# Kernel tuning notes

Hardware: AMD Instinct MI355X
Metric: run time of the kernel (lower is better)

The kernel has to match this reference:

```python
import jax, jax.numpy as jnp
import numpy as np

NUM_HEADS = 8
NEG_INF = -1e30  # stand-in for float('-inf') in masked_fill; avoids NaN rows under autodiff
LN_EPS = 1e-5


def setup_inputs() -> dict:
    key = jax.random.key(0)
    ks = jax.random.split(key, 12)
    B, C, H, W = 1, 256, 64, 64
    N = H * W
    s = 1.0 / np.sqrt(C)
    inp = {
        'x': jax.random.normal(ks[0], (B, C, H, W), jnp.float32),
        'mask': jax.random.uniform(ks[1], (B, NUM_HEADS, N, N)) < 0.5,
        'Wq': jax.random.normal(ks[2], (C, C), jnp.float32) * s,
        'bq': jax.random.normal(ks[3], (C,), jnp.float32) * 0.02,
        'Wk': jax.random.normal(ks[4], (C, C), jnp.float32) * s,
        'bk': jax.random.normal(ks[5], (C,), jnp.float32) * 0.02,
        'Wv': jax.random.normal(ks[6], (C, C), jnp.float32) * s,
        'bv': jax.random.normal(ks[7], (C,), jnp.float32) * 0.02,
        'Wo': jax.random.normal(ks[8], (C, C), jnp.float32) * s,
        'bo': jax.random.normal(ks[9], (C,), jnp.float32) * 0.02,
        'gamma': jnp.ones((C,), jnp.float32),
        'beta': jnp.zeros((C,), jnp.float32),
    }
    return inp


def reference(x, mask, Wq, bq, Wk, bk, Wv, bv, Wo, bo, gamma, beta):
    B, C, H, W = x.shape
    hd = C // NUM_HEADS
    N = H * W
    scale = hd ** -0.5

    def proj(Wm, bm):
        # 1x1 conv == per-pixel channel matmul; reshape to (B, heads, N, head_dim)
        y = jnp.einsum('oc,bchw->bohw', Wm, x) + bm[None, :, None, None]
        return y.reshape(B, NUM_HEADS, hd, N).swapaxes(2, 3)

    q = proj(Wq, bq)
    k = proj(Wk, bk)
    v = proj(Wv, bv)

    scores = jnp.einsum('bhnd,bhmd->bhnm', q, k) * scale  # (B, heads, N, N)
    scores = jnp.where(mask, scores, NEG_INF)
    probs = jax.nn.softmax(scores, axis=-1)
    # dropout is identity in eval mode
    out = jnp.einsum('bhnm,bhmd->bhnd', probs, v)
    out = out.swapaxes(2, 3).reshape(B, C, H, W)
    out = jnp.einsum('oc,bchw->bohw', Wo, out) + bo[None, :, None, None]

    z = (x + out).transpose(0, 2, 3, 1)  # (B, H, W, C) for channel-last LayerNorm
    mu = jnp.mean(z, axis=-1, keepdims=True)
    var = jnp.var(z, axis=-1, keepdims=True)
    z = (z - mu) * jax.lax.rsqrt(var + LN_EPS) * gamma + beta
    return z.transpose(0, 3, 1, 2)
```

## Files before the change

### kernel.cpp

```cpp
#include <hip/hip_runtime.h>


#define NH 8
#define CC 256
#define NN 4096
#define HD 32
#define KSPLIT 4

typedef short bf16x8 __attribute__((ext_vector_type(8)));
typedef float f32x4 __attribute__((ext_vector_type(4)));
typedef float float4v __attribute__((ext_vector_type(4)));

__device__ __forceinline__ unsigned short f2bf(float f) {
    union { float f; unsigned int i; } v;
    v.f = f;
    unsigned int i = v.i;
    i += 0x7FFFu + ((i >> 16) & 1u);
    return (unsigned short)(i >> 16);
}

__global__ __launch_bounds__(256) void proj_kernel(
    const float* __restrict__ x,
    const float* __restrict__ Wq, const float* __restrict__ bq,
    const float* __restrict__ Wk, const float* __restrict__ bk,
    const float* __restrict__ Wv, const float* __restrict__ bv,
    unsigned short* __restrict__ Qb,
    unsigned short* __restrict__ Kb,
    unsigned short* __restrict__ Vtb)
{
    const int t = threadIdx.x;
    const int which = blockIdx.y;
    const int n0 = blockIdx.x * 32;

    const float* W    = (which == 0) ? Wq : (which == 1) ? Wk : Wv;
    const float* bias = (which == 0) ? bq : (which == 1) ? bk : bv;

    __shared__ float xs[CC][36];
    {
        const float* xr = x + (size_t)t * NN + n0;
        #pragma unroll
        for (int g = 0; g < 8; ++g)
            *(float4v*)&xs[t][g * 4] = *(const float4v*)(xr + g * 4);
    }
    __syncthreads();

    float acc[32];
    #pragma unroll
    for (int i = 0; i < 32; ++i) acc[i] = 0.f;

    const float4v* w4p = (const float4v*)(W + (size_t)t * CC);
    for (int cg = 0; cg < 64; ++cg) {
        float4v w4 = w4p[cg];
        #pragma unroll
        for (int k = 0; k < 4; ++k) {
            const float w = w4[k];
            const float* xr = &xs[cg * 4 + k][0];
            #pragma unroll
            for (int g = 0; g < 8; ++g) {
                float4v xv = *(const float4v*)(xr + g * 4);
                acc[g * 4 + 0] = fmaf(w, xv[0], acc[g * 4 + 0]);
                acc[g * 4 + 1] = fmaf(w, xv[1], acc[g * 4 + 1]);
                acc[g * 4 + 2] = fmaf(w, xv[2], acc[g * 4 + 2]);
                acc[g * 4 + 3] = fmaf(w, xv[3], acc[g * 4 + 3]);
            }
        }
    }

    const float b = bias[t];
    if (which < 2) {
        unsigned short* dst = (which == 0) ? Qb : Kb;
        const int h = t >> 5, d = t & 31;
        #pragma unroll
        for (int n = 0; n < 32; ++n)
            dst[((size_t)(h * NN + n0 + n)) * HD + d] = f2bf(acc[n] + b);
    } else {
        unsigned short* dst = Vtb + (size_t)t * NN + n0;
        #pragma unroll
        for (int g = 0; g < 4; ++g) {
            unsigned short v[8];
            #pragma unroll
            for (int k = 0; k < 8; ++k) v[k] = f2bf(acc[g * 8 + k] + b);
            *(bf16x8*)(void*)(dst + g * 8) = *(const bf16x8*)(const void*)v;
        }
    }
}

__global__ __launch_bounds__(256) void flash_kernel(
    const unsigned short* __restrict__ Q,
    const unsigned short* __restrict__ K,
    const unsigned short* __restrict__ Vt,
    const int* __restrict__ mask,
    float* __restrict__ att,
    float* __restrict__ lp)
{
    const int tid  = threadIdx.x;
    const int wave = tid >> 6;
    const int lane = tid & 63;
    const int quad = lane >> 4;
    const int l16  = lane & 15;
    const int h    = blockIdx.y;
    const int ks   = blockIdx.z;
    const int q0   = blockIdx.x * 64 + wave * 16;

    float* attp = att + (size_t)ks * CC * NN;
    float* lpp  = lp  + (size_t)ks * NH * NN;

    __shared__ __align__(16) unsigned short plds[4][16 * 40];
    unsigned short* pw = plds[wave];

    const bf16x8 aq =
        *(const bf16x8*)(const void*)(Q + ((size_t)(h * NN + q0 + l16)) * HD + quad * 8);

    const unsigned short* kbase = K + (size_t)h * NN * HD;
    const unsigned short* vb0p  = Vt + ((size_t)(h * HD + l16)) * NN;
    const unsigned short* vb1p  = vb0p + (size_t)16 * NN;

    const int* mrow[4];
    #pragma unroll
    for (int r = 0; r < 4; ++r)
        mrow[r] = mask + ((size_t)(h * NN + q0 + quad * 4 + r)) * NN + l16;

    f32x4 O0 = {0.f, 0.f, 0.f, 0.f};
    f32x4 O1 = {0.f, 0.f, 0.f, 0.f};
    float l_[4] = {0.f, 0.f, 0.f, 0.f};

    const float cs = 0.25503372600239960f;
    const float c8 = 11.541560327111707f;
    const f32x4 zero4 = {0.f, 0.f, 0.f, 0.f};

    const int kbeg = ks * (NN / KSPLIT);
    const int kend = kbeg + (NN / KSPLIT);

    #pragma unroll 2
    for (int j0 = kbeg; j0 < kend; j0 += 32) {
        bf16x8 bk0 = *(const bf16x8*)(const void*)(kbase + (size_t)(j0 + l16) * HD + quad * 8);
        bf16x8 bk1 = *(const bf16x8*)(const void*)(kbase + (size_t)(j0 + 16 + l16) * HD + quad * 8);
        bf16x8 bv0 = *(const bf16x8*)(const void*)(vb0p + j0 + quad * 8);
        bf16x8 bv1 = *(const bf16x8*)(const void*)(vb1p + j0 + quad * 8);
        int mk0[4], mk1[4];
        #pragma unroll
        for (int r = 0; r < 4; ++r) { mk0[r] = mrow[r][j0]; mk1[r] = mrow[r][j0 + 16]; }

        f32x4 S0 = __builtin_amdgcn_mfma_f32_16x16x32_bf16(aq, bk0, zero4, 0, 0, 0);
        f32x4 S1 = __builtin_amdgcn_mfma_f32_16x16x32_bf16(aq, bk1, zero4, 0, 0, 0);

        #pragma unroll
        for (int r = 0; r < 4; ++r) {
            float t0 = S0[r] * cs - c8;  if (!mk0[r]) t0 = -1e38f;
            float t1 = S1[r] * cs - c8;  if (!mk1[r]) t1 = -1e38f;
            const float p0 = exp2f(t0);
            const float p1 = exp2f(t1);
            l_[r] += p0 + p1;
            pw[(quad * 4 + r) * 40 + l16]      = f2bf(p0);
            pw[(quad * 4 + r) * 40 + 16 + l16] = f2bf(p1);
        }

        __asm__ volatile("s_waitcnt lgkmcnt(0)" ::: "memory");
        bf16x8 ap = *(const bf16x8*)(const void*)(pw + l16 * 40 + quad * 8);

        O0 = __builtin_amdgcn_mfma_f32_16x16x32_bf16(ap, bv0, O0, 0, 0, 0);
        O1 = __builtin_amdgcn_mfma_f32_16x16x32_bf16(ap, bv1, O1, 0, 0, 0);
    }

    #pragma unroll
    for (int r = 0; r < 4; ++r) {
        float l = l_[r];
        l += __shfl_xor(l, 1);
        l += __shfl_xor(l, 2);
        l += __shfl_xor(l, 4);
        l += __shfl_xor(l, 8);
        const int n = q0 + quad * 4 + r;
        attp[(size_t)(h * HD + l16) * NN + n]      = O0[r];
        attp[(size_t)(h * HD + 16 + l16) * NN + n] = O1[r];
        if (l16 == 0) lpp[h * NN + n] = l;
    }
}

__global__ __launch_bounds__(256) void outln_kernel(
    const float* __restrict__ att,
    const float* __restrict__ lp,
    const float* __restrict__ x,
    const float* __restrict__ Wo,
    const float* __restrict__ bo,
    const float* __restrict__ gamma,
    const float* __restrict__ beta,
    float* __restrict__ out)
{
    const int t  = threadIdx.x;
    const int n0 = blockIdx.x * 16;

    __shared__ float as_[CC][20];
    __shared__ float red[2][16][16];
    __shared__ float mus[16], rstds[16];
    __shared__ float linv[NH][16];

    if (t < NH * 16) {
        const int h = t >> 4, nl = t & 15;
        float L = 0.f;
        #pragma unroll
        for (int s = 0; s < KSPLIT; ++s)
            L += lp[(size_t)s * NH * NN + h * NN + n0 + nl];
        linv[h][nl] = 1.f / fmaxf(L, 1e-20f);
    }
    __syncthreads();

    {
        const int h = t >> 5;
        #pragma unroll
        for (int g = 0; g < 4; ++g) {
            float4v v = {0.f, 0.f, 0.f, 0.f};
            #pragma unroll
            for (int s = 0; s < KSPLIT; ++s) {
                float4v vs = *(const float4v*)(att + (size_t)s * CC * NN
                                               + (size_t)t * NN + n0 + g * 4);
                v[0] += vs[0]; v[1] += vs[1]; v[2] += vs[2]; v[3] += vs[3];
            }
            v[0] *= linv[h][g * 4 + 0];
            v[1] *= linv[h][g * 4 + 1];
            v[2] *= linv[h][g * 4 + 2];
            v[3] *= linv[h][g * 4 + 3];
            *(float4v*)&as_[t][g * 4] = v;
        }
    }
    __syncthreads();

    float acc[16];
    #pragma unroll
    for (int i = 0; i < 16; ++i) acc[i] = 0.f;

    const float4v* w4p = (const float4v*)(Wo + (size_t)t * CC);
    for (int cg = 0; cg < 64; ++cg) {
        float4v w4 = w4p[cg];
        #pragma unroll
        for (int k = 0; k < 4; ++k) {
            const float w = w4[k];
            const float* xr = &as_[cg * 4 + k][0];
            #pragma unroll
            for (int g = 0; g < 4; ++g) {
                float4v xv = *(const float4v*)(xr + g * 4);
                acc[g * 4 + 0] = fmaf(w, xv[0], acc[g * 4 + 0]);
                acc[g * 4 + 1] = fmaf(w, xv[1], acc[g * 4 + 1]);
                acc[g * 4 + 2] = fmaf(w, xv[2], acc[g * 4 + 2]);
                acc[g * 4 + 3] = fmaf(w, xv[3], acc[g * 4 + 3]);
            }
        }
    }

    {
        const float b = bo[t];
        const float* xr = x + (size_t)t * NN + n0;
        #pragma unroll
        for (int g = 0; g < 4; ++g) {
            float4v xv = *(const float4v*)(xr + g * 4);
            acc[g * 4 + 0] += b + xv[0];
            acc[g * 4 + 1] += b + xv[1];
            acc[g * 4 + 2] += b + xv[2];
            acc[g * 4 + 3] += b + xv[3];
        }
    }

    __syncthreads();
    #pragma unroll
    for (int g = 0; g < 4; ++g) {
        float4v v = {acc[g * 4 + 0], acc[g * 4 + 1], acc[g * 4 + 2], acc[g * 4 + 3]};
        *(float4v*)&as_[t][g * 4] = v;
    }
    __syncthreads();

    {
        const int part = t >> 4, p = t & 15;
        float sm = 0.f, sq = 0.f;
        #pragma unroll
        for (int s = 0; s < 16; ++s) {
            float z = as_[part * 16 + s][p];
            sm += z;
            sq = fmaf(z, z, sq);
        }
        red[0][part][p] = sm;
        red[1][part][p] = sq;
    }
    __syncthreads();
    if (t < 16) {
        float S = 0.f, Q2 = 0.f;
        #pragma unroll
        for (int s = 0; s < 16; ++s) { S += red[0][s][t]; Q2 += red[1][s][t]; }
        const float mu  = S * (1.f / 256.f);
        const float var = Q2 * (1.f / 256.f) - mu * mu;
        mus[t]   = mu;
        rstds[t] = rsqrtf(fmaxf(var, 0.f) + 1e-5f);
    }
    __syncthreads();

    const float g_ = gamma[t];
    const float be = beta[t];
    float* dst = out + (size_t)t * NN + n0;
    #pragma unroll
    for (int g = 0; g < 4; ++g) {
        float4v v;
        v[0] = (acc[g * 4 + 0] - mus[g * 4 + 0]) * rstds[g * 4 + 0] * g_ + be;
        v[1] = (acc[g * 4 + 1] - mus[g * 4 + 1]) * rstds[g * 4 + 1] * g_ + be;
        v[2] = (acc[g * 4 + 2] - mus[g * 4 + 2]) * rstds[g * 4 + 2] * g_ + be;
        v[3] = (acc[g * 4 + 3] - mus[g * 4 + 3]) * rstds[g * 4 + 3] * g_ + be;
        *(float4v*)(dst + g * 4) = v;
    }
}

extern "C" void kernel_launch(void* const* d_in, const int* in_sizes, int n_in,
                              void* d_out, int out_size, void* d_ws, size_t ws_size,
                              hipStream_t stream) {
    const float* x     = (const float*)d_in[0];
    const int*   mask  = (const int*)d_in[1];
    const float* Wq    = (const float*)d_in[2];
    const float* bq    = (const float*)d_in[3];
    const float* Wk    = (const float*)d_in[4];
    const float* bk    = (const float*)d_in[5];
    const float* Wv    = (const float*)d_in[6];
    const float* bv    = (const float*)d_in[7];
    const float* Wo    = (const float*)d_in[8];
    const float* bo    = (const float*)d_in[9];
    const float* gamma = (const float*)d_in[10];
    const float* beta  = (const float*)d_in[11];

    char* ws = (char*)d_ws;
    unsigned short* Qb  = (unsigned short*)ws;
    unsigned short* Kb  = Qb + (size_t)NH * NN * HD;
    unsigned short* Vtb = Kb + (size_t)NH * NN * HD;
    float*          att = (float*)(Vtb + (size_t)NH * NN * HD);
    float*          lpt = att + (size_t)KSPLIT * CC * NN;

    proj_kernel<<<dim3(NN / 32, 3), 256, 0, stream>>>(x, Wq, bq, Wk, bk, Wv, bv,
                                                      Qb, Kb, Vtb);
    flash_kernel<<<dim3(NN / 64, NH, KSPLIT), 256, 0, stream>>>(Qb, Kb, Vtb,
                                                                mask, att, lpt);
    outln_kernel<<<dim3(NN / 16), 256, 0, stream>>>(att, lpt, x, Wo, bo,
                                                    gamma, beta, (float*)d_out);
}
```

Before: 836.9 us.

## Store partial attention outputs in bf16 and halve the key split

The flash kernel now writes its per-split partial outputs as bf16 instead of fp32, and the number of key splits drops from 4 to 2. The output/LayerNorm kernel reads the bf16 partials with 8-wide vector loads and converts them to float. This cuts the intermediate write and read traffic between the two kernels. In exchange the flash grid has half as many blocks, each walking twice as many keys, and the partials lose precision. The stores stay scalar 2-byte writes.

```diff
diff --git a/kernel.cpp b/kernel.cpp
--- a/kernel.cpp
+++ b/kernel.cpp
@@ -5,12 +5,18 @@
 #define CC 256
 #define NN 4096
 #define HD 32
-#define KSPLIT 4
+#define KSPLIT 2
 
 typedef short bf16x8 __attribute__((ext_vector_type(8)));
 typedef float f32x4 __attribute__((ext_vector_type(4)));
 typedef float float4v __attribute__((ext_vector_type(4)));
-
+typedef unsigned short ushort8 __attribute__((ext_vector_type(8)));
+
+__device__ __forceinline__ float bf2f(unsigned short u) {
+    union { unsigned int i; float f; } v;
+    v.i = ((unsigned int)u) << 16;
+    return v.f;
+}
 __device__ __forceinline__ unsigned short f2bf(float f) {
     union { float f; unsigned int i; } v;
     v.f = f;
@@ -90,7 +96,7 @@
     const unsigned short* __restrict__ K,
     const unsigned short* __restrict__ Vt,
     const int* __restrict__ mask,
-    float* __restrict__ att,
+    unsigned short* __restrict__ att,
     float* __restrict__ lp)
 {
     const int tid  = threadIdx.x;
@@ -102,8 +108,8 @@
     const int ks   = blockIdx.z;
     const int q0   = blockIdx.x * 64 + wave * 16;
 
-    float* attp = att + (size_t)ks * CC * NN;
-    float* lpp  = lp  + (size_t)ks * NH * NN;
+    unsigned short* attp = att + (size_t)ks * CC * NN;
+    float*          lpp  = lp  + (size_t)ks * NH * NN;
 
     __shared__ __align__(16) unsigned short plds[4][16 * 40];
     unsigned short* pw = plds[wave];
@@ -170,14 +176,14 @@
         l += __shfl_xor(l, 4);
         l += __shfl_xor(l, 8);
         const int n = q0 + quad * 4 + r;
-        attp[(size_t)(h * HD + l16) * NN + n]      = O0[r];
-        attp[(size_t)(h * HD + 16 + l16) * NN + n] = O1[r];
+        attp[(size_t)(h * HD + l16) * NN + n]      = f2bf(O0[r]);
+        attp[(size_t)(h * HD + 16 + l16) * NN + n] = f2bf(O1[r]);
         if (l16 == 0) lpp[h * NN + n] = l;
     }
 }
 
 __global__ __launch_bounds__(256) void outln_kernel(
-    const float* __restrict__ att,
+    const unsigned short* __restrict__ att,
     const float* __restrict__ lp,
     const float* __restrict__ x,
     const float* __restrict__ Wo,
@@ -207,19 +213,18 @@
     {
         const int h = t >> 5;
         #pragma unroll
-        for (int g = 0; g < 4; ++g) {
-            float4v v = {0.f, 0.f, 0.f, 0.f};
+        for (int g = 0; g < 2; ++g) {
+            float v[8] = {0.f,0.f,0.f,0.f,0.f,0.f,0.f,0.f};
             #pragma unroll
             for (int s = 0; s < KSPLIT; ++s) {
-                float4v vs = *(const float4v*)(att + (size_t)s * CC * NN
-                                               + (size_t)t * NN + n0 + g * 4);
-                v[0] += vs[0]; v[1] += vs[1]; v[2] += vs[2]; v[3] += vs[3];
+                ushort8 vs = *(const ushort8*)(const void*)
+                    (att + (size_t)s * CC * NN + (size_t)t * NN + n0 + g * 8);
+                #pragma unroll
+                for (int k = 0; k < 8; ++k) v[k] += bf2f(vs[k]);
             }
-            v[0] *= linv[h][g * 4 + 0];
-            v[1] *= linv[h][g * 4 + 1];
-            v[2] *= linv[h][g * 4 + 2];
-            v[3] *= linv[h][g * 4 + 3];
-            *(float4v*)&as_[t][g * 4] = v;
+            #pragma unroll
+            for (int k = 0; k < 8; ++k)
+                as_[t][g * 8 + k] = v[k] * linv[h][g * 8 + k];
         }
     }
     __syncthreads();
@@ -325,8 +330,8 @@
     unsigned short* Qb  = (unsigned short*)ws;
     unsigned short* Kb  = Qb + (size_t)NH * NN * HD;
     unsigned short* Vtb = Kb + (size_t)NH * NN * HD;
-    float*          att = (float*)(Vtb + (size_t)NH * NN * HD);
-    float*          lpt = att + (size_t)KSPLIT * CC * NN;
+    unsigned short* att = Vtb + (size_t)NH * NN * HD;
+    float*          lpt = (float*)(att + (size_t)KSPLIT * CC * NN);
 
     proj_kernel<<<dim3(NN / 32, 3), 256, 0, stream>>>(x, Wq, bq, Wk, bk, Wv, bv,
                                                       Qb, Kb, Vtb);
```

Result: no change. 833.1 us (-0.5%).
